# Kernel optimization log

Measured on AMD Instinct MI355X. Metric: run time of the kernel, lower is better.

## Reference

```python
import jax, jax.numpy as jnp
import numpy as np

B, T, D, H = 8, 2048, 1024, 128


def setup_inputs() -> dict:
    key = jax.random.key(0)
    k1, k2, k3, k4 = jax.random.split(key, 4)
    x = jax.random.normal(k1, (B, T, D), dtype=jnp.float32)
    # nn.Linear(D, H, bias=False): y = x @ W.T with W [H, D]; we store W as [D, H]
    Wq = jax.random.normal(k2, (D, H), dtype=jnp.float32) * (1.0 / np.sqrt(D))
    Wk = jax.random.normal(k3, (D, H), dtype=jnp.float32) * (1.0 / np.sqrt(D))
    Wv = jax.random.normal(k4, (D, H), dtype=jnp.float32) * (1.0 / np.sqrt(D))
    return {"x": x, "Wq": Wq, "Wk": Wk, "Wv": Wv}


def reference(x, Wq, Wk, Wv):
    # q, k, v projections (bias-free)
    q = jnp.einsum("btd,dh->bth", x, Wq)
    k = jnp.einsum("btd,dh->bth", x, Wk)
    v = jnp.einsum("btd,dh->bth", x, Wv)
    scale = 1.0 / jnp.sqrt(jnp.asarray(q.shape[-1], dtype=q.dtype))
    # full T x T score matrix, as in the original module
    scores = jnp.einsum("bqh,bkh->bqk", q, k) * scale
    T_ = x.shape[1]
    causal = jnp.tril(jnp.ones((T_, T_), dtype=bool))
    scores = jnp.where(causal[None, :, :], scores, -jnp.inf)
    weights = jax.nn.softmax(scores, axis=-1)
    # dropout is identity in eval mode (deterministic reference)
    return jnp.einsum("bqk,bkh->bqh", weights, v)
```

## Files before the change

### kernel.cpp

```cpp
#include <hip/hip_runtime.h>

typedef float  f32x4  __attribute__((ext_vector_type(4)));
typedef __bf16 bf16x8 __attribute__((ext_vector_type(8)));
typedef unsigned short u16;
typedef unsigned int   u32;
typedef u32 u32x4 __attribute__((ext_vector_type(4)));
typedef u16 u16x4 __attribute__((ext_vector_type(4)));
typedef u16 u16x8 __attribute__((ext_vector_type(8)));
typedef float f32x4v __attribute__((ext_vector_type(4)));

#define B_ 8
#define T_ 2048
#define D_ 1024
#define H_ 128
#define M_ (B_ * T_)

__device__ __forceinline__ u16 f2b(float f) {
  u32 u = __builtin_bit_cast(u32, f);
  u32 r = u + 0x7fffu + ((u >> 16) & 1u);
  return (u16)(r >> 16);
}

__device__ __forceinline__ void gl2lds16(const void* g, void* l) {
  __builtin_amdgcn_global_load_lds(
      (const __attribute__((address_space(1))) void*)g,
      (__attribute__((address_space(3))) void*)l, 16, 0, 0);
}

__global__ __launch_bounds__(256) void wt_kernel(const float* __restrict__ Wq,
                                                 const float* __restrict__ Wk,
                                                 const float* __restrict__ Wv,
                                                 u16* __restrict__ ws) {
  __shared__ u16 Ld[32 * 136];
  const float* W = (blockIdx.y == 0) ? Wq : (blockIdx.y == 1) ? Wk : Wv;
  u16* Wt = ws + (size_t)blockIdx.y * (D_ * H_);
  const int d0 = blockIdx.x * 32;
  const int t = threadIdx.x;
  for (int i = 0; i < 4; ++i) {
    int idx = i * 256 + t;
    int d = idx >> 5, h4 = (idx & 31) * 4;
    f32x4v wv = *(const f32x4v*)(W + (size_t)(d0 + d) * H_ + h4);
    u16x4 bv;
    bv[0] = f2b(wv[0]); bv[1] = f2b(wv[1]); bv[2] = f2b(wv[2]); bv[3] = f2b(wv[3]);
    *(u16x4*)(&Ld[d * 136 + h4]) = bv;
  }
  __syncthreads();
  for (int i = 0; i < 2; ++i) {
    int idx = i * 256 + t;
    int h = idx >> 2, d8 = (idx & 3) * 8;
    u16x8 ov;
    for (int j = 0; j < 8; ++j) ov[j] = Ld[(d8 + j) * 136 + h];
    *(u16x8*)(Wt + (size_t)h * D_ + d0 + d8) = ov;
  }
}

__global__ __launch_bounds__(512, 4) void qkv_gemm(const float* __restrict__ x,
                                                   const u16* __restrict__ Wt_all,
                                                   u16* __restrict__ Qb,
                                                   u16* __restrict__ Kb,
                                                   u16* __restrict__ Vt) {
  __shared__ __attribute__((aligned(16))) u16 As[2][64 * 40];
  __shared__ __attribute__((aligned(16))) u16 Bs[2][192 * 32];
  const int m0 = (int)(blockIdx.x >> 1) * 64;
  const int n0 = (int)(blockIdx.x & 1) * 192;
  const int t = threadIdx.x;
  const int lane = t & 63;
  const int w = t >> 6;
  const int wm = (w & 1) * 32, wn = (w >> 1) * 48;
  const int li = lane & 15, q4 = lane >> 4;
  const int arow = t >> 3, ac4 = (t & 7) * 4;
  const int br = lane >> 2, bu = lane & 3;
  const int bul = bu ^ ((br >> 1) & 3);

  f32x4 acc[2][3];
  for (int i = 0; i < 2; ++i)
    for (int j = 0; j < 3; ++j) acc[i][j] = (f32x4){0.f, 0.f, 0.f, 0.f};

  f32x4v areg;
  auto load_a = [&](int kt) {
    areg = *(const f32x4v*)(x + (size_t)(m0 + arow) * D_ + kt * 32 + ac4);
  };
  auto stage_b = [&](int kt, int sb) {
    for (int ii = 0; ii < 2; ++ii) {
      int seg = ii * 8 + w;
      if (seg < 12)
        gl2lds16(Wt_all + (size_t)(n0 + seg * 16 + br) * D_ + kt * 32 + bul * 8,
                 &Bs[sb][seg * 512]);
    }
  };

  load_a(0);
  stage_b(0, 0);
  for (int kt = 0; kt < 32; ++kt) {
    const int s = kt & 1;
    {
      u16x4 av;
      av[0] = f2b(areg[0]); av[1] = f2b(areg[1]);
      av[2] = f2b(areg[2]); av[3] = f2b(areg[3]);
      *(u16x4*)(&As[s][arow * 40 + ac4]) = av;
    }
    __syncthreads();
    if (kt + 1 < 32) { load_a(kt + 1); stage_b(kt + 1, s ^ 1); }

    bf16x8 af[2];
    for (int i = 0; i < 2; ++i)
      af[i] = *(const bf16x8*)(&As[s][(wm + i * 16 + li) * 40 + q4 * 8]);
    for (int j = 0; j < 3; ++j) {
      int R = wn + j * 16 + li;
      bf16x8 bfr = *(const bf16x8*)(&Bs[s][R * 32 + (q4 ^ ((li >> 1) & 3)) * 8]);
      for (int i = 0; i < 2; ++i)
        acc[i][j] = __builtin_amdgcn_mfma_f32_16x16x32_bf16(af[i], bfr, acc[i][j], 0, 0, 0);
    }
  }

  const float qs = 0.12751740696864213f;
  const int bb = m0 >> 11;
  const int tl0 = (m0 & (T_ - 1)) + wm + q4 * 4;
  for (int j = 0; j < 3; ++j) {
    int n = n0 + wn + j * 16 + li;
    int p = n >> 7, col = n & 127;
    if (p == 2) {
      for (int i = 0; i < 2; ++i) {
        u16x4 pv;
        for (int r = 0; r < 4; ++r) pv[r] = f2b(acc[i][j][r]);
        *(u16x4*)(Vt + (size_t)bb * (H_ * T_) + (size_t)col * T_ + tl0 + i * 16) = pv;
      }
    } else {
      u16* dst = (p == 0) ? Qb : Kb;
      float sc = (p == 0) ? qs : 1.0f;
      for (int i = 0; i < 2; ++i)
        for (int r = 0; r < 4; ++r) {
          int mg = m0 + wm + i * 16 + q4 * 4 + r;
          dst[(size_t)mg * H_ + col] = f2b(acc[i][j][r] * sc);
        }
    }
  }
}

#define NSLOT_PER_B 36

__device__ __forceinline__ int slot_base(int qt) {
  return (qt < 8) ? 2 * (qt - 4) : (qt < 12) ? 8 + 3 * (qt - 8) : 20 + 4 * (qt - 12);
}

__global__ __launch_bounds__(512, 2) void flash_split(const u16* __restrict__ Qb,
                                                      const u16* __restrict__ Kb,
                                                      const u16* __restrict__ Vt,
                                                      float* __restrict__ Opart,
                                                      float* __restrict__ Ls,
                                                      float* __restrict__ out) {
  __shared__ __attribute__((aligned(16))) u16 Ks[2][64 * 128];
  __shared__ __attribute__((aligned(16))) u16 Vs[2][128 * 64];
  __shared__ __attribute__((aligned(16))) u16 Ps[128 * 72];

  int xb = blockIdx.x, qt = 15, split = 0;
  for (int q = 15; q >= 0; --q) {
    int ns = (2 * q + 9) >> 3;
    if (xb < ns) { qt = q; split = xb; break; }
    xb -= ns;
  }
  const int b = blockIdx.y;
  const int nkv = 2 * qt + 2;
  const int nsplit = (2 * qt + 9) >> 3;
  const int kv0t = split * 8;
  const int kv1t = (kv0t + 8 < nkv) ? kv0t + 8 : nkv;
  const int q0 = qt * 128;

  const int t = threadIdx.x;
  const int lane = t & 63;
  const int w = t >> 6;
  const int li = lane & 15, q4 = lane >> 4;

  bf16x8 qf[4];
  const int qrow = b * T_ + q0 + w * 16 + li;
  for (int kk = 0; kk < 4; ++kk)
    qf[kk] = *(const bf16x8*)(Qb + (size_t)qrow * H_ + kk * 32 + q4 * 8);

  f32x4 oacc[8];
  for (int i = 0; i < 8; ++i) oacc[i] = (f32x4){0.f, 0.f, 0.f, 0.f};
  float rs[4] = {0.f, 0.f, 0.f, 0.f};

  auto stage = [&](int jt, int sb) {
    const int j0 = jt * 64;
    for (int i = 0; i < 2; ++i) {
      int seg = i * 8 + w;
      {
        int r = seg * 4 + (lane >> 4);
        int c = (lane & 15) ^ (r & 7);
        gl2lds16(Kb + (size_t)(b * T_ + j0 + r) * H_ + c * 8, &Ks[sb][seg << 9]);
      }
      {
        int r = seg * 8 + (lane >> 3);
        int c = (lane & 7) ^ (r & 7);
        gl2lds16(Vt + (size_t)b * (H_ * T_) + (size_t)r * T_ + j0 + c * 8,
                 &Vs[sb][seg << 9]);
      }
    }
  };

  stage(kv0t, 0);
  for (int jt = kv0t; jt < kv1t; ++jt) {
    const int buf = (jt - kv0t) & 1;
    const int j0 = jt * 64;
    __syncthreads();
    if (jt + 1 < kv1t) stage(jt + 1, buf ^ 1);

    f32x4 sacc[4];
    for (int jn = 0; jn < 4; ++jn) sacc[jn] = (f32x4){0.f, 0.f, 0.f, 0.f};
    for (int jn = 0; jn < 4; ++jn) {
      int row = jn * 16 + li;
      for (int kk = 0; kk < 4; ++kk) {
        int phys = ((kk << 2) | q4) ^ (row & 7);
        bf16x8 kf = *(const bf16x8*)(&Ks[buf][row * 128 + phys * 8]);
        sacc[jn] = __builtin_amdgcn_mfma_f32_16x16x32_bf16(qf[kk], kf, sacc[jn], 0, 0, 0);
      }
    }

    if (jt >= 2 * qt) {
      for (int jn = 0; jn < 4; ++jn) {
        int jg = j0 + jn * 16 + li;
        for (int r = 0; r < 4; ++r) {
          int qg = q0 + w * 16 + q4 * 4 + r;
          if (jg > qg) sacc[jn][r] = -1e30f;
        }
      }
    }

    for (int jn = 0; jn < 4; ++jn)
      for (int r = 0; r < 4; ++r) {
        float p = exp2f(sacc[jn][r]);
        rs[r] += p;
        Ps[(w * 16 + q4 * 4 + r) * 72 + jn * 16 + li] = f2b(p);
      }

    for (int ks = 0; ks < 2; ++ks) {
      bf16x8 pa = *(const bf16x8*)(&Ps[(w * 16 + li) * 72 + ks * 32 + q4 * 8]);
      for (int hn = 0; hn < 8; ++hn) {
        int row = hn * 16 + li;
        int phys = ((ks << 2) | q4) ^ (row & 7);
        bf16x8 vf = *(const bf16x8*)(&Vs[buf][row * 64 + phys * 8]);
        oacc[hn] = __builtin_amdgcn_mfma_f32_16x16x32_bf16(pa, vf, oacc[hn], 0, 0, 0);
      }
    }
  }

  float lr[4];
  for (int r = 0; r < 4; ++r) {
    float s = rs[r];
    for (int off = 1; off < 16; off <<= 1) s += __shfl_xor(s, off, 16);
    lr[r] = s;
  }

  if (nsplit == 1) {
    for (int hn = 0; hn < 8; ++hn)
      for (int r = 0; r < 4; ++r) {
        int qg = b * T_ + q0 + w * 16 + q4 * 4 + r;
        out[(size_t)qg * H_ + hn * 16 + li] = oacc[hn][r] / lr[r];
      }
  } else {
    const int slot = b * NSLOT_PER_B + slot_base(qt) + split;
    float* Od = Opart + (size_t)slot * (128 * 128);
    for (int hn = 0; hn < 8; ++hn)
      for (int r = 0; r < 4; ++r) {
        int qq = w * 16 + q4 * 4 + r;
        Od[qq * 128 + hn * 16 + li] = oacc[hn][r];
      }
    if (li == 0)
      for (int r = 0; r < 4; ++r)
        Ls[slot * 128 + w * 16 + q4 * 4 + r] = lr[r];
  }
}

__global__ __launch_bounds__(512) void flash_merge(const float* __restrict__ Opart,
                                                   const float* __restrict__ Ls,
                                                   float* __restrict__ out) {
  __shared__ float inv_l[128];
  const int qt = 4 + blockIdx.x;
  const int b = blockIdx.y;
  const int nsplit = (2 * qt + 9) >> 3;
  const int slot0 = b * NSLOT_PER_B + slot_base(qt);
  const int t = threadIdx.x;

  if (t < 128) {
    float L = 0.f;
    for (int s = 0; s < nsplit; ++s) L += Ls[(slot0 + s) * 128 + t];
    inv_l[t] = 1.0f / L;
  }
  __syncthreads();

  float* dst = out + ((size_t)b * T_ + (size_t)qt * 128) * H_;
  for (int i = 0; i < 8; ++i) {
    int e4 = i * 512 + t;
    int q = e4 >> 5;
    f32x4 acc = (f32x4){0.f, 0.f, 0.f, 0.f};
    for (int s = 0; s < nsplit; ++s) {
      f32x4 v = *(const f32x4*)(Opart + (size_t)(slot0 + s) * (128 * 128) + e4 * 4);
      acc[0] += v[0]; acc[1] += v[1]; acc[2] += v[2]; acc[3] += v[3];
    }
    float inv = inv_l[q];
    acc[0] *= inv; acc[1] *= inv; acc[2] *= inv; acc[3] *= inv;
    *(f32x4*)(dst + e4 * 4) = acc;
  }
}

extern "C" void kernel_launch(void* const* d_in, const int* in_sizes, int n_in,
                              void* d_out, int out_size, void* d_ws, size_t ws_size,
                              hipStream_t stream) {
  const float* x  = (const float*)d_in[0];
  const float* Wq = (const float*)d_in[1];
  const float* Wk = (const float*)d_in[2];
  const float* Wv = (const float*)d_in[3];
  float* out = (float*)d_out;

  u16* ws = (u16*)d_ws;
  u16* WtAll = ws;
  u16* Qb = ws + 3 * (size_t)(D_ * H_);
  u16* Kb = Qb + (size_t)M_ * H_;
  u16* Vt = Kb + (size_t)M_ * H_;
  float* Opart = (float*)(Vt + (size_t)M_ * H_);
  float* Ls = Opart + (size_t)8 * NSLOT_PER_B * 128 * 128;

  wt_kernel<<<dim3(32, 3), 256, 0, stream>>>(Wq, Wk, Wv, WtAll);
  qkv_gemm<<<dim3(512), 512, 0, stream>>>(x, WtAll, Qb, Kb, Vt);
  flash_split<<<dim3(40, 8), 512, 0, stream>>>(Qb, Kb, Vt, Opart, Ls, out);
  flash_merge<<<dim3(12, 8), 512, 0, stream>>>(Opart, Ls, out);
}
```

Before: 179.2 us.

## Double QKV GEMM K-tile to 64, swizzle B and P in LDS, raise flash occupancy

The QKV projection GEMM now stages a K-slice of 64 per iteration instead of 32. That halves the main-loop trip count and the number of barriers, and uses an XOR swizzle on the weight tile in shared memory. The flash kernel replaces the padded P buffer with an XOR-swizzled layout that shrinks its LDS footprint, and asks for 4 blocks per CU instead of 2. The higher launch bound could force register spills, and the LDS total (about 80 KB per block) may not fit four blocks per CU, so the occupancy hint might have no effect.

Result: faster. 161.7 us (-9.8%).

```diff
diff --git a/kernel.cpp b/kernel.cpp
--- a/kernel.cpp
+++ b/kernel.cpp
@@ -59,8 +59,8 @@
                                                    u16* __restrict__ Qb,
                                                    u16* __restrict__ Kb,
                                                    u16* __restrict__ Vt) {
-  __shared__ __attribute__((aligned(16))) u16 As[2][64 * 40];
-  __shared__ __attribute__((aligned(16))) u16 Bs[2][192 * 32];
+  __shared__ __attribute__((aligned(16))) u16 As[2][64 * 72];
+  __shared__ __attribute__((aligned(16))) u16 Bs[2][192 * 64];
   const int m0 = (int)(blockIdx.x >> 1) * 64;
   const int n0 = (int)(blockIdx.x & 1) * 192;
   const int t = threadIdx.x;
@@ -68,48 +68,52 @@
   const int w = t >> 6;
   const int wm = (w & 1) * 32, wn = (w >> 1) * 48;
   const int li = lane & 15, q4 = lane >> 4;
-  const int arow = t >> 3, ac4 = (t & 7) * 4;
-  const int br = lane >> 2, bu = lane & 3;
-  const int bul = bu ^ ((br >> 1) & 3);
+  const int arow = t >> 3, ac0 = (t & 7) * 4;
+  const int brr = lane >> 3, bp = lane & 7;
 
   f32x4 acc[2][3];
   for (int i = 0; i < 2; ++i)
     for (int j = 0; j < 3; ++j) acc[i][j] = (f32x4){0.f, 0.f, 0.f, 0.f};
 
-  f32x4v areg;
+  f32x4v areg[2];
   auto load_a = [&](int kt) {
-    areg = *(const f32x4v*)(x + (size_t)(m0 + arow) * D_ + kt * 32 + ac4);
+    for (int ii = 0; ii < 2; ++ii)
+      areg[ii] = *(const f32x4v*)(x + (size_t)(m0 + arow) * D_ + kt * 64 + ac0 + ii * 32);
   };
   auto stage_b = [&](int kt, int sb) {
-    for (int ii = 0; ii < 2; ++ii) {
-      int seg = ii * 8 + w;
-      if (seg < 12)
-        gl2lds16(Wt_all + (size_t)(n0 + seg * 16 + br) * D_ + kt * 32 + bul * 8,
-                 &Bs[sb][seg * 512]);
+    for (int s3 = 0; s3 < 3; ++s3) {
+      int seg = s3 * 8 + w;
+      int r = seg * 8 + brr;
+      int u = bp ^ (r & 7);
+      gl2lds16(Wt_all + (size_t)(n0 + r) * D_ + kt * 64 + u * 8,
+               &Bs[sb][seg * 512]);
     }
   };
 
   load_a(0);
   stage_b(0, 0);
-  for (int kt = 0; kt < 32; ++kt) {
+  for (int kt = 0; kt < 16; ++kt) {
     const int s = kt & 1;
-    {
+    for (int ii = 0; ii < 2; ++ii) {
       u16x4 av;
-      av[0] = f2b(areg[0]); av[1] = f2b(areg[1]);
-      av[2] = f2b(areg[2]); av[3] = f2b(areg[3]);
-      *(u16x4*)(&As[s][arow * 40 + ac4]) = av;
+      av[0] = f2b(areg[ii][0]); av[1] = f2b(areg[ii][1]);
+      av[2] = f2b(areg[ii][2]); av[3] = f2b(areg[ii][3]);
+      *(u16x4*)(&As[s][arow * 72 + ac0 + ii * 32]) = av;
     }
     __syncthreads();
-    if (kt + 1 < 32) { load_a(kt + 1); stage_b(kt + 1, s ^ 1); }
-
-    bf16x8 af[2];
-    for (int i = 0; i < 2; ++i)
-      af[i] = *(const bf16x8*)(&As[s][(wm + i * 16 + li) * 40 + q4 * 8]);
-    for (int j = 0; j < 3; ++j) {
-      int R = wn + j * 16 + li;
-      bf16x8 bfr = *(const bf16x8*)(&Bs[s][R * 32 + (q4 ^ ((li >> 1) & 3)) * 8]);
+    if (kt + 1 < 16) { load_a(kt + 1); stage_b(kt + 1, s ^ 1); }
+
+    for (int kk = 0; kk < 2; ++kk) {
+      bf16x8 af[2];
       for (int i = 0; i < 2; ++i)
-        acc[i][j] = __builtin_amdgcn_mfma_f32_16x16x32_bf16(af[i], bfr, acc[i][j], 0, 0, 0);
+        af[i] = *(const bf16x8*)(&As[s][(wm + i * 16 + li) * 72 + kk * 32 + q4 * 8]);
+      for (int j = 0; j < 3; ++j) {
+        int R = wn + j * 16 + li;
+        int phys = ((kk << 2) | q4) ^ (R & 7);
+        bf16x8 bfr = *(const bf16x8*)(&Bs[s][R * 64 + phys * 8]);
+        for (int i = 0; i < 2; ++i)
+          acc[i][j] = __builtin_amdgcn_mfma_f32_16x16x32_bf16(af[i], bfr, acc[i][j], 0, 0, 0);
+      }
     }
   }
 
@@ -143,7 +147,7 @@
   return (qt < 8) ? 2 * (qt - 4) : (qt < 12) ? 8 + 3 * (qt - 8) : 20 + 4 * (qt - 12);
 }
 
-__global__ __launch_bounds__(512, 2) void flash_split(const u16* __restrict__ Qb,
+__global__ __launch_bounds__(512, 4) void flash_split(const u16* __restrict__ Qb,
                                                       const u16* __restrict__ Kb,
                                                       const u16* __restrict__ Vt,
                                                       float* __restrict__ Opart,
@@ -151,7 +155,7 @@
                                                       float* __restrict__ out) {
   __shared__ __attribute__((aligned(16))) u16 Ks[2][64 * 128];
   __shared__ __attribute__((aligned(16))) u16 Vs[2][128 * 64];
-  __shared__ __attribute__((aligned(16))) u16 Ps[128 * 72];
+  __shared__ __attribute__((aligned(16))) u16 Ps[128 * 64];
 
   int xb = blockIdx.x, qt = 15, split = 0;
   for (int q = 15; q >= 0; --q) {
@@ -230,11 +234,15 @@
       for (int r = 0; r < 4; ++r) {
         float p = exp2f(sacc[jn][r]);
         rs[r] += p;
-        Ps[(w * 16 + q4 * 4 + r) * 72 + jn * 16 + li] = f2b(p);
+        int row = w * 16 + q4 * 4 + r;
+        int col = jn * 16 + li;
+        Ps[row * 64 + ((col >> 3) ^ (row & 7)) * 8 + (col & 7)] = f2b(p);
       }
 
     for (int ks = 0; ks < 2; ++ks) {
-      bf16x8 pa = *(const bf16x8*)(&Ps[(w * 16 + li) * 72 + ks * 32 + q4 * 8]);
+      int prow = w * 16 + li;
+      int pphys = ((ks << 2) | q4) ^ (prow & 7);
+      bf16x8 pa = *(const bf16x8*)(&Ps[prow * 64 + pphys * 8]);
       for (int hn = 0; hn < 8; ++hn) {
         int row = hn * 16 + li;
         int phys = ((ks << 2) | q4) ^ (row & 7);
```
